# Kernel tuning notes

Hardware: AMD Instinct MI355X
Metric: run time of the kernel (lower is better)

## Reference

```python
import jax, jax.numpy as jnp
import numpy as np

A, B, I, H, O = 400, 64, 50, 192, 3   # num_agents, batch, input_dim, hidden_dim, output_dim
ADIM, NH = 128, 8                      # attention_dim, num_heads
HD = ADIM // NH
SCALE = HD ** -0.5
EPS = 1e-5


def _ln(x, g, b):
    mu = jnp.mean(x, -1, keepdims=True)
    v = jnp.mean((x - mu) ** 2, -1, keepdims=True)
    return (x - mu) * jax.lax.rsqrt(v + EPS) * g + b


def setup_inputs() -> dict:
    key = jax.random.key(0)
    ks = jax.random.split(key, 12)
    s = 0.05
    n = lambda k, shape: (jax.random.normal(k, shape, jnp.float32) * s)
    return {
        'x': jax.random.normal(ks[0], (B, I), jnp.float32),
        'ln_in_g': jnp.ones((A, I), jnp.float32), 'ln_in_b': jnp.zeros((A, I), jnp.float32),
        'W1': n(ks[1], (A, I, H)), 'b1': jnp.zeros((A, H), jnp.float32),
        'Ws1': n(ks[2], (A, I, H)), 'bs1': jnp.zeros((A, H), jnp.float32),
        'W2': n(ks[3], (A, H, H)), 'b2': jnp.zeros((A, H), jnp.float32),
        'Ws2': n(ks[4], (A, H, H)), 'bs2': jnp.zeros((A, H), jnp.float32),
        'W3': n(ks[5], (A, H, H)), 'b3': jnp.zeros((A, H), jnp.float32),
        'ln_h_g': jnp.ones((A, H), jnp.float32), 'ln_h_b': jnp.zeros((A, H), jnp.float32),
        'Wout': n(ks[6], (A, H, O)), 'bout': jnp.zeros((A, O), jnp.float32),
        'aln_g': jnp.ones((H,), jnp.float32), 'aln_b': jnp.zeros((H,), jnp.float32),
        'Wq': n(ks[7], (H, ADIM)), 'bq': jnp.zeros((ADIM,), jnp.float32),
        'Wk': n(ks[8], (H, ADIM)), 'bk': jnp.zeros((ADIM,), jnp.float32),
        'Wv': n(ks[9], (H, ADIM)), 'bv': jnp.zeros((ADIM,), jnp.float32),
        'Wo': n(ks[10], (ADIM, H)), 'bo': jnp.zeros((H,), jnp.float32),
    }


def _forward(x, ln_in_g, ln_in_b, W1, b1, Ws1, bs1, W2, b2, Ws2, bs2, W3, b3,
             ln_h_g, ln_h_b, Wout, bout, aln_g, aln_b, Wq, bq, Wk, bk, Wv, bv, Wo, bo):
    gelu = lambda t: jax.nn.gelu(t, approximate=False)  # torch F.gelu default = exact erf
    # per-agent input LayerNorm (shared stats, per-agent affine) -> [A, B, I]
    xn = _ln(x[None, :, :], ln_in_g[:, None, :], ln_in_b[:, None, :])
    # agent MLPs as batched GEMMs over agent axis
    h1 = gelu(jnp.einsum('abi,aih->abh', xn, W1) + b1[:, None, :]) \
         + jnp.einsum('abi,aih->abh', xn, Ws1) + bs1[:, None, :]
    h2 = gelu(jnp.einsum('abh,ahk->abk', h1, W2) + b2[:, None, :]) \
         + jnp.einsum('abh,ahk->abk', h1, Ws2) + bs2[:, None, :]
    h3 = _ln(h2 + jnp.einsum('abh,ahk->abk', h2, W3) + b3[:, None, :],
             ln_h_g[:, None, :], ln_h_b[:, None, :])  # [A, B, H]
    # cross-SREK attention across the agent axis
    y = _ln(h3, aln_g, aln_b)
    q = (y @ Wq + bq).reshape(A, B, NH, HD).transpose(1, 2, 0, 3)  # [B, NH, A, HD]
    k = (y @ Wk + bk).reshape(A, B, NH, HD).transpose(1, 2, 0, 3)
    v = (y @ Wv + bv).reshape(A, B, NH, HD).transpose(1, 2, 0, 3)
    attn = jax.nn.softmax(jnp.einsum('bhad,bhcd->bhac', q, k) * SCALE, axis=-1)
    o = jnp.einsum('bhac,bhcd->bhad', attn, v).transpose(2, 0, 1, 3).reshape(A, B, ADIM)
    attended = h3 + (o @ Wo + bo)  # residual (dropout off in eval)
    # per-agent output heads -> [A, B, O]
    logits = jnp.einsum('abh,aho->abo', attended, Wout) + bout[:, None, :]
    return logits


def reference(x, ln_in_g, ln_in_b, W1, b1, Ws1, bs1, W2, b2, Ws2, bs2, W3, b3,
              ln_h_g, ln_h_b, Wout, bout, aln_g, aln_b, Wq, bq, Wk, bk, Wv, bv, Wo, bo):
    return _forward(x, ln_in_g, ln_in_b, W1, b1, Ws1, bs1, W2, b2, Ws2, bs2, W3, b3,
                    ln_h_g, ln_h_b, Wout, bout, aln_g, aln_b, Wq, bq, Wk, bk, Wv, bv, Wo, bo)
```

## Files before the change

### kernel.cpp

```cpp
#include <hip/hip_runtime.h>
#include <math.h>

#define AGENTS 400
#define BATCH  64
#define IDIM   50
#define HDIM   192
#define ODIM   3
#define ADIMM  128
#define NHEADS 8
#define HEADD  16
#define LN_EPS 1e-5f

#define PA 200

typedef __bf16 bf16x8 __attribute__((ext_vector_type(8)));
typedef float  f32x4  __attribute__((ext_vector_type(4)));

__device__ __forceinline__ float gelu_exact(float x) {
    return 0.5f * x * (1.0f + erff(x * 0.70710678118654752f));
}

template<int NC, int KD, int NT, int LDW>
__device__ __forceinline__ void gemm_bpass(f32x4 (&acc)[4][NT],
                                           const float* const* wptr,
                                           const __bf16* Asrc, int lane)
{
    const int r = lane & 15, g = lane >> 4;
    float buf[2][NT * 8];

    #pragma unroll
    for (int t = 0; t < NT; t++)
        #pragma unroll
        for (int j = 0; j < 8; j++) {
            int k = g * 8 + j;
            buf[0][t * 8 + j] = (k < KD) ? wptr[t][k * LDW + r] : 0.f;
        }

    #pragma unroll
    for (int c = 0; c < NC; c++) {
        const int cur = c & 1, nxt = cur ^ 1;
        if (c + 1 < NC) {
            #pragma unroll
            for (int t = 0; t < NT; t++)
                #pragma unroll
                for (int j = 0; j < 8; j++) {
                    int k = (c + 1) * 32 + g * 8 + j;
                    buf[nxt][t * 8 + j] = (k < KD) ? wptr[t][k * LDW + r] : 0.f;
                }
        }
        bf16x8 bfr[NT];
        #pragma unroll
        for (int t = 0; t < NT; t++)
            #pragma unroll
            for (int j = 0; j < 8; j++)
                bfr[t][j] = (__bf16)buf[cur][t * 8 + j];
        #pragma unroll
        for (int rg = 0; rg < 4; rg++) {
            bf16x8 af = *(const bf16x8*)&Asrc[(16 * rg + r) * PA + c * 32 + g * 8];
            #pragma unroll
            for (int t = 0; t < NT; t++)
                acc[rg][t] = __builtin_amdgcn_mfma_f32_16x16x32_bf16(af, bfr[t], acc[rg][t], 0, 0, 0);
        }
    }
}

__global__ __launch_bounds__(256, 2) void mlp_kernel(
    const float* __restrict__ x,
    const float* __restrict__ ln_in_g, const float* __restrict__ ln_in_b,
    const float* __restrict__ W1, const float* __restrict__ b1,
    const float* __restrict__ Ws1, const float* __restrict__ bs1,
    const float* __restrict__ W2, const float* __restrict__ b2,
    const float* __restrict__ Ws2, const float* __restrict__ bs2,
    const float* __restrict__ W3, const float* __restrict__ b3,
    const float* __restrict__ ln_h_g, const float* __restrict__ ln_h_b,
    float* __restrict__ h3out)
{
    const int a    = blockIdx.x;
    const int tid  = threadIdx.x;
    const int wave = tid >> 6, lane = tid & 63;
    const int r = lane & 15, g = lane >> 4;
    const int n0 = 48 * wave;

    __shared__ __align__(16) __bf16 As[64 * PA];
    __shared__ float mu_s[64], rs_s[64];

    {
        int rr = tid >> 2, l = tid & 3;
        float s = 0.f, ss = 0.f;
        for (int k = l; k < IDIM; k += 4) { float v = x[rr * IDIM + k]; s += v; ss += v * v; }
        s  += __shfl_down(s, 2, 4);  s  += __shfl_down(s, 1, 4);
        ss += __shfl_down(ss, 2, 4); ss += __shfl_down(ss, 1, 4);
        if (l == 0) {
            float mu = s * (1.0f / IDIM);
            float var = ss * (1.0f / IDIM) - mu * mu;
            mu_s[rr] = mu;
            rs_s[rr] = rsqrtf(var + LN_EPS);
        }
    }
    __syncthreads();
    for (int sidx = tid; sidx < 64 * 64; sidx += 256) {
        int rr = sidx >> 6, k = sidx & 63;
        float v = 0.f;
        if (k < IDIM)
            v = (x[rr * IDIM + k] - mu_s[rr]) * rs_s[rr] * ln_in_g[a * IDIM + k] + ln_in_b[a * IDIM + k];
        As[rr * PA + k] = (__bf16)v;
    }
    __syncthreads();

    {
        f32x4 acc1[4][3], acc2[4][3];
        #pragma unroll
        for (int i = 0; i < 4; i++)
            #pragma unroll
            for (int t = 0; t < 3; t++) { acc1[i][t] = (f32x4)0.f; acc2[i][t] = (f32x4)0.f; }
        const float* W1p  = W1  + (size_t)a * IDIM * HDIM;
        const float* Ws1p = Ws1 + (size_t)a * IDIM * HDIM;
        const float* wA[3] = { W1p + n0,  W1p + n0 + 16,  W1p + n0 + 32 };
        const float* wB[3] = { Ws1p + n0, Ws1p + n0 + 16, Ws1p + n0 + 32 };
        gemm_bpass<2, IDIM, 3, HDIM>(acc1, wA, As, lane);
        gemm_bpass<2, IDIM, 3, HDIM>(acc2, wB, As, lane);
        __syncthreads();
        #pragma unroll
        for (int t = 0; t < 3; t++) {
            int col = n0 + 16 * t + r;
            float bb  = b1[a * HDIM + col];
            float bbs = bs1[a * HDIM + col];
            #pragma unroll
            for (int rg = 0; rg < 4; rg++)
                #pragma unroll
                for (int i = 0; i < 4; i++) {
                    int row = 16 * rg + 4 * g + i;
                    float v = gelu_exact(acc1[rg][t][i] + bb) + acc2[rg][t][i] + bbs;
                    As[row * PA + col] = (__bf16)v;
                }
        }
        __syncthreads();
    }

    {
        f32x4 acc1[4][3], acc2[4][3];
        #pragma unroll
        for (int i = 0; i < 4; i++)
            #pragma unroll
            for (int t = 0; t < 3; t++) { acc1[i][t] = (f32x4)0.f; acc2[i][t] = (f32x4)0.f; }
        const float* W2p  = W2  + (size_t)a * HDIM * HDIM;
        const float* Ws2p = Ws2 + (size_t)a * HDIM * HDIM;
        const float* wA[3] = { W2p + n0,  W2p + n0 + 16,  W2p + n0 + 32 };
        const float* wB[3] = { Ws2p + n0, Ws2p + n0 + 16, Ws2p + n0 + 32 };
        gemm_bpass<6, HDIM, 3, HDIM>(acc1, wA, As, lane);
        gemm_bpass<6, HDIM, 3, HDIM>(acc2, wB, As, lane);
        __syncthreads();
        #pragma unroll
        for (int t = 0; t < 3; t++) {
            int col = n0 + 16 * t + r;
            float bb  = b2[a * HDIM + col];
            float bbs = bs2[a * HDIM + col];
            #pragma unroll
            for (int rg = 0; rg < 4; rg++)
                #pragma unroll
                for (int i = 0; i < 4; i++) {
                    int row = 16 * rg + 4 * g + i;
                    float v = gelu_exact(acc1[rg][t][i] + bb) + acc2[rg][t][i] + bbs;
                    As[row * PA + col] = (__bf16)v;
                }
        }
        __syncthreads();
    }

    {
        f32x4 acc[4][3];
        #pragma unroll
        for (int i = 0; i < 4; i++)
            #pragma unroll
            for (int t = 0; t < 3; t++) acc[i][t] = (f32x4)0.f;
        const float* W3p = W3 + (size_t)a * HDIM * HDIM;
        const float* wA[3] = { W3p + n0, W3p + n0 + 16, W3p + n0 + 32 };
        gemm_bpass<6, HDIM, 3, HDIM>(acc, wA, As, lane);
        __syncthreads();
        #pragma unroll
        for (int t = 0; t < 3; t++) {
            int col = n0 + 16 * t + r;
            float bb = b3[a * HDIM + col];
            #pragma unroll
            for (int rg = 0; rg < 4; rg++)
                #pragma unroll
                for (int i = 0; i < 4; i++) {
                    int row = 16 * rg + 4 * g + i;
                    float v = (float)As[row * PA + col] + acc[rg][t][i] + bb;
                    As[row * PA + col] = (__bf16)v;
                }
        }
        __syncthreads();
    }

    {
        int rr = tid >> 2, l = tid & 3;
        float s = 0.f, ss = 0.f;
        for (int k = l; k < HDIM; k += 4) { float v = (float)As[rr * PA + k]; s += v; ss += v * v; }
        s  += __shfl_down(s, 2, 4);  s  += __shfl_down(s, 1, 4);
        ss += __shfl_down(ss, 2, 4); ss += __shfl_down(ss, 1, 4);
        if (l == 0) {
            float mu = s * (1.0f / HDIM);
            float var = ss * (1.0f / HDIM) - mu * mu;
            mu_s[rr] = mu;
            rs_s[rr] = rsqrtf(var + LN_EPS);
        }
    }
    __syncthreads();
    for (int sidx = tid; sidx < 64 * HDIM; sidx += 256) {
        int rr = sidx / HDIM, c = sidx - rr * HDIM;
        float v = ((float)As[rr * PA + c] - mu_s[rr]) * rs_s[rr] * ln_h_g[a * HDIM + c] + ln_h_b[a * HDIM + c];
        h3out[((size_t)a * BATCH + rr) * HDIM + c] = v;
    }
}

__global__ __launch_bounds__(256, 2) void qkv_kernel(
    const float* __restrict__ h3,
    const float* __restrict__ aln_g, const float* __restrict__ aln_b,
    const float* __restrict__ Wq, const float* __restrict__ bq,
    const float* __restrict__ Wk, const float* __restrict__ bk,
    const float* __restrict__ Wv, const float* __restrict__ bv,
    float* __restrict__ qT, float* __restrict__ kT, float* __restrict__ vT)
{
    const int a    = blockIdx.x;
    const int tid  = threadIdx.x;
    const int wave = tid >> 6, lane = tid & 63;
    const int r = lane & 15, g = lane >> 4;

    __shared__ __align__(16) __bf16 ys[64 * PA];
    __shared__ float mu_s[64], rs_s[64];

    {
        int rr = tid >> 2, l = tid & 3;
        const float* hp = h3 + ((size_t)a * BATCH + rr) * HDIM;
        float s = 0.f, ss = 0.f;
        for (int k = l; k < HDIM; k += 4) { float v = hp[k]; s += v; ss += v * v; }
        s  += __shfl_down(s, 2, 4);  s  += __shfl_down(s, 1, 4);
        ss += __shfl_down(ss, 2, 4); ss += __shfl_down(ss, 1, 4);
        if (l == 0) {
            float mu = s * (1.0f / HDIM);
            float var = ss * (1.0f / HDIM) - mu * mu;
            mu_s[rr] = mu;
            rs_s[rr] = rsqrtf(var + LN_EPS);
        }
    }
    __syncthreads();
    for (int sidx = tid; sidx < 64 * HDIM; sidx += 256) {
        int rr = sidx / HDIM, c = sidx - rr * HDIM;
        float v = (h3[((size_t)a * BATCH + rr) * HDIM + c] - mu_s[rr]) * rs_s[rr] * aln_g[c] + aln_b[c];
        ys[rr * PA + c] = (__bf16)v;
    }
    __syncthreads();

    #pragma unroll
    for (int p = 0; p < 2; p++) {
        const int nb = 192 * p + 48 * wave;
        const float* wA[3];
        #pragma unroll
        for (int t = 0; t < 3; t++) {
            int nt = nb + 16 * t;
            const float* base = (nt < 128) ? Wq : (nt < 256) ? Wk : Wv;
            wA[t] = base + (nt & 127);
        }
        f32x4 acc[4][3];
        #pragma unroll
        for (int i = 0; i < 4; i++)
            #pragma unroll
            for (int t = 0; t < 3; t++) acc[i][t] = (f32x4)0.f;
        gemm_bpass<6, HDIM, 3, ADIMM>(acc, wA, ys, lane);

        #pragma unroll
        for (int t = 0; t < 3; t++) {
            int n = nb + 16 * t + r;
            int which = n >> 7, cc = n & 127, hh = cc >> 4, dd = cc & 15;
            const float* bp = (which == 0) ? bq : (which == 1) ? bk : bv;
            float* op = (which == 0) ? qT : (which == 1) ? kT : vT;
            float bb = bp[cc];
            #pragma unroll
            for (int rg = 0; rg < 4; rg++)
                #pragma unroll
                for (int i = 0; i < 4; i++) {
                    int brow = 16 * rg + 4 * g + i;
                    op[(((size_t)brow * NHEADS + hh) * AGENTS + a) * HEADD + dd] = acc[rg][t][i] + bb;
                }
        }
    }
}

#define PKA 24
#define PVA 408
#define PPA 232

__global__ __launch_bounds__(256, 2) void attn_kernel(
    const float* __restrict__ qT, const float* __restrict__ kT,
    const float* __restrict__ vT, float* __restrict__ oT)
{
    const int bh   = blockIdx.x;
    const int tid  = threadIdx.x;
    const int wave = tid >> 6, lane = tid & 63;
    const int r = lane & 15, g = lane >> 4;

    __shared__ __align__(16) __bf16 Ks[AGENTS * PKA];
    __shared__ __align__(16) __bf16 Vt[16 * PVA];
    __shared__ __align__(16) __bf16 Ps[4][16 * PPA];

    const float* kp = kT + (size_t)bh * AGENTS * HEADD;
    const float* vp = vT + (size_t)bh * AGENTS * HEADD;
    for (int idx = tid; idx < AGENTS * HEADD; idx += 256) {
        int a_ = idx >> 4, d = idx & 15;
        Ks[a_ * PKA + d] = (__bf16)kp[idx];
        Vt[d * PVA + a_] = (__bf16)vp[idx];
    }
    __bf16* Pw = Ps[wave];
    for (int z = lane; z < 16 * 16; z += 64)
        Pw[(z >> 4) * PPA + 208 + (z & 15)] = (__bf16)0.f;
    __syncthreads();

    for (int mt = wave; mt < 25; mt += 4) {
        const int m0 = mt * 16;

        bf16x8 aq;
        if (g < 2) {
            const float* qp = qT + ((size_t)bh * AGENTS + m0 + r) * HEADD + g * 8;
            #pragma unroll
            for (int j = 0; j < 8; j++) aq[j] = (__bf16)(qp[j] * 0.25f);
        } else {
            #pragma unroll
            for (int j = 0; j < 8; j++) aq[j] = (__bf16)0.f;
        }

        f32x4 sacc[25];
        #pragma unroll
        for (int t = 0; t < 25; t++) {
            bf16x8 bk_ = *(const bf16x8*)&Ks[(t * 16 + r) * PKA + (g & 1) * 8];
            sacc[t] = __builtin_amdgcn_mfma_f32_16x16x32_bf16(aq, bk_, (f32x4)0.f, 0, 0, 0);
        }

        float lv[4];
        #pragma unroll
        for (int i = 0; i < 4; i++) {
            float m_ = sacc[0][i];
            #pragma unroll
            for (int t = 1; t < 25; t++) m_ = fmaxf(m_, sacc[t][i]);
            #pragma unroll
            for (int off = 8; off; off >>= 1) m_ = fmaxf(m_, __shfl_xor(m_, off, 16));
            float l_ = 0.f;
            #pragma unroll
            for (int t = 0; t < 25; t++) {
                float p = __expf(sacc[t][i] - m_);
                sacc[t][i] = p;
                l_ += p;
            }
            #pragma unroll
            for (int off = 8; off; off >>= 1) l_ += __shfl_xor(l_, off, 16);
            lv[i] = l_;
        }

        f32x4 oacc = (f32x4)0.f;

        #pragma unroll
        for (int t = 0; t < 13; t++)
            #pragma unroll
            for (int i = 0; i < 4; i++)
                Pw[(g * 4 + i) * PPA + t * 16 + r] = (__bf16)sacc[t][i];
        __asm__ volatile("s_waitcnt lgkmcnt(0)" ::: "memory");
        #pragma unroll
        for (int c = 0; c < 7; c++) {
            bf16x8 ap  = *(const bf16x8*)&Pw[r * PPA + c * 32 + g * 8];
            bf16x8 bv_ = *(const bf16x8*)&Vt[r * PVA + c * 32 + g * 8];
            oacc = __builtin_amdgcn_mfma_f32_16x16x32_bf16(ap, bv_, oacc, 0, 0, 0);
        }

        for (int z = lane; z < 16 * 16; z += 64)
            Pw[(z >> 4) * PPA + 192 + (z & 15)] = (__bf16)0.f;
        #pragma unroll
        for (int t = 13; t < 25; t++)
            #pragma unroll
            for (int i = 0; i < 4; i++)
                Pw[(g * 4 + i) * PPA + (t - 13) * 16 + r] = (__bf16)sacc[t][i];
        __asm__ volatile("s_waitcnt lgkmcnt(0)" ::: "memory");
        #pragma unroll
        for (int c = 0; c < 6; c++) {
            bf16x8 ap  = *(const bf16x8*)&Pw[r * PPA + c * 32 + g * 8];
            bf16x8 bv_ = *(const bf16x8*)&Vt[r * PVA + 208 + c * 32 + g * 8];
            oacc = __builtin_amdgcn_mfma_f32_16x16x32_bf16(ap, bv_, oacc, 0, 0, 0);
        }

        float* op = oT + ((size_t)bh * AGENTS + m0) * HEADD;
        #pragma unroll
        for (int i = 0; i < 4; i++)
            op[(g * 4 + i) * HEADD + r] = oacc[i] / lv[i];
    }
}

__global__ __launch_bounds__(256) void out_kernel(
    const float* __restrict__ h3, const float* __restrict__ oT,
    const float* __restrict__ Wo, const float* __restrict__ bo,
    const float* __restrict__ Wout, const float* __restrict__ bout,
    float* __restrict__ out)
{
    const int a      = blockIdx.x;
    const int r_base = blockIdx.y * 32;
    const int tid    = threadIdx.x;
    __shared__ float os[32][ADIMM + 1];
    __shared__ float att[32][HDIM + 1];

    for (int idx = tid; idx < 32 * HDIM; idx += 256) {
        int rr = idx / HDIM, c = idx - rr * HDIM;
        att[rr][c] = h3[((size_t)a * BATCH + (r_base + rr)) * HDIM + c];
    }
    for (int idx = tid; idx < 32 * ADIMM; idx += 256) {
        int rr = idx >> 7, j = idx & 127;
        int h = j >> 4, d = j & 15;
        int b = r_base + rr;
        os[rr][j] = oT[(((size_t)b * NHEADS + h) * AGENTS + a) * HEADD + d];
    }
    __syncthreads();

    const int cx = tid & 63;
    const int rg = (tid >> 6) * 8;
    {
        float acc[3][8];
        #pragma unroll
        for (int m = 0; m < 3; m++)
            #pragma unroll
            for (int rr = 0; rr < 8; rr++) acc[m][rr] = 0.f;
        for (int k = 0; k < ADIMM; k++) {
            float w[3];
            #pragma unroll
            for (int m = 0; m < 3; m++) w[m] = Wo[k * HDIM + cx + 64 * m];
            #pragma unroll
            for (int rr = 0; rr < 8; rr++) {
                float ov = os[rg + rr][k];
                #pragma unroll
                for (int m = 0; m < 3; m++) acc[m][rr] = fmaf(ov, w[m], acc[m][rr]);
            }
        }
        #pragma unroll
        for (int m = 0; m < 3; m++) {
            int c = cx + 64 * m;
            float bb = bo[c];
            #pragma unroll
            for (int rr = 0; rr < 8; rr++)
                att[rg + rr][c] += acc[m][rr] + bb;
        }
    }
    __syncthreads();

    if (tid < 32 * ODIM) {
        int rr = tid & 31;
        int c = tid >> 5;
        const float* Wp = Wout + (size_t)a * HDIM * ODIM;
        float accv = 0.f;
        for (int k = 0; k < HDIM; k++)
            accv = fmaf(att[rr][k], Wp[k * ODIM + c], accv);
        out[((size_t)a * BATCH + (r_base + rr)) * ODIM + c] = accv + bout[a * ODIM + c];
    }
}

extern "C" void kernel_launch(void* const* d_in, const int* in_sizes, int n_in,
                              void* d_out, int out_size, void* d_ws, size_t ws_size,
                              hipStream_t stream)
{
    const float* x       = (const float*)d_in[0];
    const float* ln_in_g = (const float*)d_in[1];
    const float* ln_in_b = (const float*)d_in[2];
    const float* W1      = (const float*)d_in[3];
    const float* b1      = (const float*)d_in[4];
    const float* Ws1     = (const float*)d_in[5];
    const float* bs1     = (const float*)d_in[6];
    const float* W2      = (const float*)d_in[7];
    const float* b2      = (const float*)d_in[8];
    const float* Ws2     = (const float*)d_in[9];
    const float* bs2     = (const float*)d_in[10];
    const float* W3      = (const float*)d_in[11];
    const float* b3      = (const float*)d_in[12];
    const float* ln_h_g  = (const float*)d_in[13];
    const float* ln_h_b  = (const float*)d_in[14];
    const float* Wout    = (const float*)d_in[15];
    const float* bout    = (const float*)d_in[16];
    const float* aln_g   = (const float*)d_in[17];
    const float* aln_b   = (const float*)d_in[18];
    const float* Wq      = (const float*)d_in[19];
    const float* bq      = (const float*)d_in[20];
    const float* Wk      = (const float*)d_in[21];
    const float* bk      = (const float*)d_in[22];
    const float* Wv      = (const float*)d_in[23];
    const float* bv      = (const float*)d_in[24];
    const float* Wo      = (const float*)d_in[25];
    const float* bo      = (const float*)d_in[26];
    float* out = (float*)d_out;

    float* ws = (float*)d_ws;
    const size_t H3_SZ = (size_t)AGENTS * BATCH * HDIM;
    const size_t QT_SZ = (size_t)BATCH * NHEADS * AGENTS * HEADD;
    float* h3 = ws;
    float* qT = h3 + H3_SZ;
    float* kT = qT + QT_SZ;
    float* vT = kT + QT_SZ;
    float* oT = vT + QT_SZ;

    mlp_kernel<<<AGENTS, 256, 0, stream>>>(x, ln_in_g, ln_in_b,
                                           W1, b1, Ws1, bs1, W2, b2, Ws2, bs2,
                                           W3, b3, ln_h_g, ln_h_b, h3);
    qkv_kernel<<<AGENTS, 256, 0, stream>>>(h3, aln_g, aln_b,
                                           Wq, bq, Wk, bk, Wv, bv, qT, kT, vT);
    attn_kernel<<<BATCH * NHEADS, 256, 0, stream>>>(qT, kT, vT, oT);
    out_kernel<<<dim3(AGENTS, 2), 256, 0, stream>>>(h3, oT, Wo, bo, Wout, bout, out);
}
```

Before: 400.7 us.

## Double waves per block in MLP/QKV and move output projection to MFMA

The MLP and QKV kernels now launch 512 threads, splitting the 64 batch rows into two halves across wave pairs, so each wave holds half the accumulators and more waves hide weight-load latency. The attention kernel now writes its output in agent-major [A,B,ADIM] order so the output kernel can read contiguous rows. The output kernel is rewritten to do the Wo projection and the per-agent Wout head with bf16 MFMA instead of scalar FMA loops, using one block per agent. Each weight tile is now loaded by twice as many waves, and the extra bf16 rounding of the residual before the head may cost some accuracy.

```diff
diff --git a/kernel.cpp b/kernel.cpp
--- a/kernel.cpp
+++ b/kernel.cpp
@@ -11,7 +11,8 @@
 #define HEADD  16
 #define LN_EPS 1e-5f
 
-#define PA 200
+#define PA   200
+#define POUT 136
 
 typedef __bf16 bf16x8 __attribute__((ext_vector_type(8)));
 typedef float  f32x4  __attribute__((ext_vector_type(4)));
@@ -20,8 +21,14 @@
     return 0.5f * x * (1.0f + erff(x * 0.70710678118654752f));
 }
 
-template<int NC, int KD, int NT, int LDW>
-__device__ __forceinline__ void gemm_bpass(f32x4 (&acc)[4][NT],
+__device__ __forceinline__ unsigned pack_bf16x2(float a, float b) {
+    unsigned short ua = __builtin_bit_cast(unsigned short, (__bf16)a);
+    unsigned short ub = __builtin_bit_cast(unsigned short, (__bf16)b);
+    return (unsigned)ua | ((unsigned)ub << 16);
+}
+
+template<int NC, int KD, int NT, int NRG, int LDW, int PITCH>
+__device__ __forceinline__ void gemm_bpass(f32x4 (&acc)[NRG][NT],
                                            const float* const* wptr,
                                            const __bf16* Asrc, int lane)
 {
@@ -55,8 +62,8 @@
             for (int j = 0; j < 8; j++)
                 bfr[t][j] = (__bf16)buf[cur][t * 8 + j];
         #pragma unroll
-        for (int rg = 0; rg < 4; rg++) {
-            bf16x8 af = *(const bf16x8*)&Asrc[(16 * rg + r) * PA + c * 32 + g * 8];
+        for (int rg = 0; rg < NRG; rg++) {
+            bf16x8 af = *(const bf16x8*)&Asrc[(16 * rg + r) * PITCH + c * 32 + g * 8];
             #pragma unroll
             for (int t = 0; t < NT; t++)
                 acc[rg][t] = __builtin_amdgcn_mfma_f32_16x16x32_bf16(af, bfr[t], acc[rg][t], 0, 0, 0);
@@ -64,7 +71,7 @@
     }
 }
 
-__global__ __launch_bounds__(256, 2) void mlp_kernel(
+__global__ __launch_bounds__(512, 4) void mlp_kernel(
     const float* __restrict__ x,
     const float* __restrict__ ln_in_g, const float* __restrict__ ln_in_b,
     const float* __restrict__ W1, const float* __restrict__ b1,
@@ -79,17 +86,23 @@
     const int tid  = threadIdx.x;
     const int wave = tid >> 6, lane = tid & 63;
     const int r = lane & 15, g = lane >> 4;
-    const int n0 = 48 * wave;
+    const int cg = wave & 3, mh = wave >> 2;
+    const int n0 = 48 * cg;
+    const __bf16* Aw;
 
     __shared__ __align__(16) __bf16 As[64 * PA];
     __shared__ float mu_s[64], rs_s[64];
-
-    {
-        int rr = tid >> 2, l = tid & 3;
+    Aw = As + 32 * mh * PA;
+
+    {
+        int rr = tid >> 3, l = tid & 7;
         float s = 0.f, ss = 0.f;
-        for (int k = l; k < IDIM; k += 4) { float v = x[rr * IDIM + k]; s += v; ss += v * v; }
-        s  += __shfl_down(s, 2, 4);  s  += __shfl_down(s, 1, 4);
-        ss += __shfl_down(ss, 2, 4); ss += __shfl_down(ss, 1, 4);
+        for (int k = l; k < IDIM; k += 8) { float v = x[rr * IDIM + k]; s += v; ss += v * v; }
+        #pragma unroll
+        for (int off = 4; off; off >>= 1) {
+            s  += __shfl_down(s,  off, 8);
+            ss += __shfl_down(ss, off, 8);
+        }
         if (l == 0) {
             float mu = s * (1.0f / IDIM);
             float var = ss * (1.0f / IDIM) - mu * mu;
@@ -98,7 +111,7 @@
         }
     }
     __syncthreads();
-    for (int sidx = tid; sidx < 64 * 64; sidx += 256) {
+    for (int sidx = tid; sidx < 64 * 64; sidx += 512) {
         int rr = sidx >> 6, k = sidx & 63;
         float v = 0.f;
         if (k < IDIM)
@@ -108,17 +121,22 @@
     __syncthreads();
 
     {
-        f32x4 acc1[4][3], acc2[4][3];
-        #pragma unroll
-        for (int i = 0; i < 4; i++)
-            #pragma unroll
-            for (int t = 0; t < 3; t++) { acc1[i][t] = (f32x4)0.f; acc2[i][t] = (f32x4)0.f; }
         const float* W1p  = W1  + (size_t)a * IDIM * HDIM;
         const float* Ws1p = Ws1 + (size_t)a * IDIM * HDIM;
         const float* wA[3] = { W1p + n0,  W1p + n0 + 16,  W1p + n0 + 32 };
         const float* wB[3] = { Ws1p + n0, Ws1p + n0 + 16, Ws1p + n0 + 32 };
-        gemm_bpass<2, IDIM, 3, HDIM>(acc1, wA, As, lane);
-        gemm_bpass<2, IDIM, 3, HDIM>(acc2, wB, As, lane);
+        f32x4 acc1[2][3];
+        #pragma unroll
+        for (int i = 0; i < 2; i++)
+            #pragma unroll
+            for (int t = 0; t < 3; t++) acc1[i][t] = (f32x4)0.f;
+        gemm_bpass<2, IDIM, 3, 2, HDIM, PA>(acc1, wA, Aw, lane);
+        f32x4 acc2[2][3];
+        #pragma unroll
+        for (int i = 0; i < 2; i++)
+            #pragma unroll
+            for (int t = 0; t < 3; t++) acc2[i][t] = (f32x4)0.f;
+        gemm_bpass<2, IDIM, 3, 2, HDIM, PA>(acc2, wB, Aw, lane);
         __syncthreads();
         #pragma unroll
         for (int t = 0; t < 3; t++) {
@@ -126,10 +144,10 @@
             float bb  = b1[a * HDIM + col];
             float bbs = bs1[a * HDIM + col];
             #pragma unroll
-            for (int rg = 0; rg < 4; rg++)
+            for (int rg = 0; rg < 2; rg++)
                 #pragma unroll
                 for (int i = 0; i < 4; i++) {
-                    int row = 16 * rg + 4 * g + i;
+                    int row = 32 * mh + 16 * rg + 4 * g + i;
                     float v = gelu_exact(acc1[rg][t][i] + bb) + acc2[rg][t][i] + bbs;
                     As[row * PA + col] = (__bf16)v;
                 }
@@ -138,17 +156,22 @@
     }
 
     {
-        f32x4 acc1[4][3], acc2[4][3];
-        #pragma unroll
-        for (int i = 0; i < 4; i++)
-            #pragma unroll
-            for (int t = 0; t < 3; t++) { acc1[i][t] = (f32x4)0.f; acc2[i][t] = (f32x4)0.f; }
         const float* W2p  = W2  + (size_t)a * HDIM * HDIM;
         const float* Ws2p = Ws2 + (size_t)a * HDIM * HDIM;
         const float* wA[3] = { W2p + n0,  W2p + n0 + 16,  W2p + n0 + 32 };
         const float* wB[3] = { Ws2p + n0, Ws2p + n0 + 16, Ws2p + n0 + 32 };
-        gemm_bpass<6, HDIM, 3, HDIM>(acc1, wA, As, lane);
-        gemm_bpass<6, HDIM, 3, HDIM>(acc2, wB, As, lane);
+        f32x4 acc1[2][3];
+        #pragma unroll
+        for (int i = 0; i < 2; i++)
+            #pragma unroll
+            for (int t = 0; t < 3; t++) acc1[i][t] = (f32x4)0.f;
+        gemm_bpass<6, HDIM, 3, 2, HDIM, PA>(acc1, wA, Aw, lane);
+        f32x4 acc2[2][3];
+        #pragma unroll
+        for (int i = 0; i < 2; i++)
+            #pragma unroll
+            for (int t = 0; t < 3; t++) acc2[i][t] = (f32x4)0.f;
+        gemm_bpass<6, HDIM, 3, 2, HDIM, PA>(acc2, wB, Aw, lane);
         __syncthreads();
         #pragma unroll
         for (int t = 0; t < 3; t++) {
@@ -156,10 +179,10 @@
             float bb  = b2[a * HDIM + col];
             float bbs = bs2[a * HDIM + col];
             #pragma unroll
-            for (int rg = 0; rg < 4; rg++)
+            for (int rg = 0; rg < 2; rg++)
                 #pragma unroll
                 for (int i = 0; i < 4; i++) {
-                    int row = 16 * rg + 4 * g + i;
+                    int row = 32 * mh + 16 * rg + 4 * g + i;
                     float v = gelu_exact(acc1[rg][t][i] + bb) + acc2[rg][t][i] + bbs;
                     As[row * PA + col] = (__bf16)v;
                 }
@@ -168,24 +191,24 @@
     }
 
     {
-        f32x4 acc[4][3];
-        #pragma unroll
-        for (int i = 0; i < 4; i++)
-            #pragma unroll
-            for (int t = 0; t < 3; t++) acc[i][t] = (f32x4)0.f;
         const float* W3p = W3 + (size_t)a * HDIM * HDIM;
         const float* wA[3] = { W3p + n0, W3p + n0 + 16, W3p + n0 + 32 };
-        gemm_bpass<6, HDIM, 3, HDIM>(acc, wA, As, lane);
+        f32x4 acc[2][3];
+        #pragma unroll
+        for (int i = 0; i < 2; i++)
+            #pragma unroll
+            for (int t = 0; t < 3; t++) acc[i][t] = (f32x4)0.f;
+        gemm_bpass<6, HDIM, 3, 2, HDIM, PA>(acc, wA, Aw, lane);
         __syncthreads();
         #pragma unroll
         for (int t = 0; t < 3; t++) {
             int col = n0 + 16 * t + r;
             float bb = b3[a * HDIM + col];
             #pragma unroll
-            for (int rg = 0; rg < 4; rg++)
+            for (int rg = 0; rg < 2; rg++)
                 #pragma unroll
                 for (int i = 0; i < 4; i++) {
-                    int row = 16 * rg + 4 * g + i;
+                    int row = 32 * mh + 16 * rg + 4 * g + i;
                     float v = (float)As[row * PA + col] + acc[rg][t][i] + bb;
                     As[row * PA + col] = (__bf16)v;
                 }
@@ -194,11 +217,14 @@
     }
 
     {
-        int rr = tid >> 2, l = tid & 3;
+        int rr = tid >> 3, l = tid & 7;
         float s = 0.f, ss = 0.f;
-        for (int k = l; k < HDIM; k += 4) { float v = (float)As[rr * PA + k]; s += v; ss += v * v; }
-        s  += __shfl_down(s, 2, 4);  s  += __shfl_down(s, 1, 4);
-        ss += __shfl_down(ss, 2, 4); ss += __shfl_down(ss, 1, 4);
+        for (int k = l; k < HDIM; k += 8) { float v = (float)As[rr * PA + k]; s += v; ss += v * v; }
+        #pragma unroll
+        for (int off = 4; off; off >>= 1) {
+            s  += __shfl_down(s,  off, 8);
+            ss += __shfl_down(ss, off, 8);
+        }
         if (l == 0) {
             float mu = s * (1.0f / HDIM);
             float var = ss * (1.0f / HDIM) - mu * mu;
@@ -207,14 +233,14 @@
         }
     }
     __syncthreads();
-    for (int sidx = tid; sidx < 64 * HDIM; sidx += 256) {
+    for (int sidx = tid; sidx < 64 * HDIM; sidx += 512) {
         int rr = sidx / HDIM, c = sidx - rr * HDIM;
         float v = ((float)As[rr * PA + c] - mu_s[rr]) * rs_s[rr] * ln_h_g[a * HDIM + c] + ln_h_b[a * HDIM + c];
         h3out[((size_t)a * BATCH + rr) * HDIM + c] = v;
     }
 }
 
-__global__ __launch_bounds__(256, 2) void qkv_kernel(
+__global__ __launch_bounds__(512, 4) void qkv_kernel(
     const float* __restrict__ h3,
     const float* __restrict__ aln_g, const float* __restrict__ aln_b,
     const float* __restrict__ Wq, const float* __restrict__ bq,
@@ -226,17 +252,22 @@
     const int tid  = threadIdx.x;
     const int wave = tid >> 6, lane = tid & 63;
     const int r = lane & 15, g = lane >> 4;
+    const int cg = wave & 3, mh = wave >> 2;
 
     __shared__ __align__(16) __bf16 ys[64 * PA];
     __shared__ float mu_s[64], rs_s[64];
-
-    {
-        int rr = tid >> 2, l = tid & 3;
+    const __bf16* Aw = ys + 32 * mh * PA;
+
+    {
+        int rr = tid >> 3, l = tid & 7;
         const float* hp = h3 + ((size_t)a * BATCH + rr) * HDIM;
         float s = 0.f, ss = 0.f;
-        for (int k = l; k < HDIM; k += 4) { float v = hp[k]; s += v; ss += v * v; }
-        s  += __shfl_down(s, 2, 4);  s  += __shfl_down(s, 1, 4);
-        ss += __shfl_down(ss, 2, 4); ss += __shfl_down(ss, 1, 4);
+        for (int k = l; k < HDIM; k += 8) { float v = hp[k]; s += v; ss += v * v; }
+        #pragma unroll
+        for (int off = 4; off; off >>= 1) {
+            s  += __shfl_down(s,  off, 8);
+            ss += __shfl_down(ss, off, 8);
+        }
         if (l == 0) {
             float mu = s * (1.0f / HDIM);
             float var = ss * (1.0f / HDIM) - mu * mu;
@@ -245,7 +276,7 @@
         }
     }
     __syncthreads();
-    for (int sidx = tid; sidx < 64 * HDIM; sidx += 256) {
+    for (int sidx = tid; sidx < 64 * HDIM; sidx += 512) {
         int rr = sidx / HDIM, c = sidx - rr * HDIM;
         float v = (h3[((size_t)a * BATCH + rr) * HDIM + c] - mu_s[rr]) * rs_s[rr] * aln_g[c] + aln_b[c];
         ys[rr * PA + c] = (__bf16)v;
@@ -254,7 +285,7 @@
 
     #pragma unroll
     for (int p = 0; p < 2; p++) {
-        const int nb = 192 * p + 48 * wave;
+        const int nb = 192 * p + 48 * cg;
         const float* wA[3];
         #pragma unroll
         for (int t = 0; t < 3; t++) {
@@ -262,12 +293,12 @@
             const float* base = (nt < 128) ? Wq : (nt < 256) ? Wk : Wv;
             wA[t] = base + (nt & 127);
         }
-        f32x4 acc[4][3];
-        #pragma unroll
-        for (int i = 0; i < 4; i++)
+        f32x4 acc[2][3];
+        #pragma unroll
+        for (int i = 0; i < 2; i++)
             #pragma unroll
             for (int t = 0; t < 3; t++) acc[i][t] = (f32x4)0.f;
-        gemm_bpass<6, HDIM, 3, ADIMM>(acc, wA, ys, lane);
+        gemm_bpass<6, HDIM, 3, 2, ADIMM, PA>(acc, wA, Aw, lane);
 
         #pragma unroll
         for (int t = 0; t < 3; t++) {
@@ -277,10 +308,10 @@
             float* op = (which == 0) ? qT : (which == 1) ? kT : vT;
             float bb = bp[cc];
             #pragma unroll
-            for (int rg = 0; rg < 4; rg++)
+            for (int rg = 0; rg < 2; rg++)
                 #pragma unroll
                 for (int i = 0; i < 4; i++) {
-                    int brow = 16 * rg + 4 * g + i;
+                    int brow = 32 * mh + 16 * rg + 4 * g + i;
                     op[(((size_t)brow * NHEADS + hh) * AGENTS + a) * HEADD + dd] = acc[rg][t][i] + bb;
                 }
         }
@@ -296,6 +327,7 @@
     const float* __restrict__ vT, float* __restrict__ oT)
 {
     const int bh   = blockIdx.x;
+    const int b    = bh >> 3, h = bh & 7;
     const int tid  = threadIdx.x;
     const int wave = tid >> 6, lane = tid & 63;
     const int r = lane & 15, g = lane >> 4;
@@ -386,75 +418,87 @@
             oacc = __builtin_amdgcn_mfma_f32_16x16x32_bf16(ap, bv_, oacc, 0, 0, 0);
         }
 
-        float* op = oT + ((size_t)bh * AGENTS + m0) * HEADD;
         #pragma unroll
         for (int i = 0; i < 4; i++)
-            op[(g * 4 + i) * HEADD + r] = oacc[i] / lv[i];
-    }
-}
-
-__global__ __launch_bounds__(256) void out_kernel(
+            oT[((size_t)(m0 + g * 4 + i) * BATCH + b) * ADIMM + h * HEADD + r] = oacc[i] / lv[i];
+    }
+}
+
+__global__ __launch_bounds__(256, 2) void out_kernel(
     const float* __restrict__ h3, const float* __restrict__ oT,
     const float* __restrict__ Wo, const float* __restrict__ bo,
     const float* __restrict__ Wout, const float* __restrict__ bout,
     float* __restrict__ out)
 {
-    const int a      = blockIdx.x;
-    const int r_base = blockIdx.y * 32;
-    const int tid    = threadIdx.x;
-    __shared__ float os[32][ADIMM + 1];
-    __shared__ float att[32][HDIM + 1];
-
-    for (int idx = tid; idx < 32 * HDIM; idx += 256) {
-        int rr = idx / HDIM, c = idx - rr * HDIM;
-        att[rr][c] = h3[((size_t)a * BATCH + (r_base + rr)) * HDIM + c];
-    }
-    for (int idx = tid; idx < 32 * ADIMM; idx += 256) {
-        int rr = idx >> 7, j = idx & 127;
-        int h = j >> 4, d = j & 15;
-        int b = r_base + rr;
-        os[rr][j] = oT[(((size_t)b * NHEADS + h) * AGENTS + a) * HEADD + d];
-    }
-    __syncthreads();
-
-    const int cx = tid & 63;
-    const int rg = (tid >> 6) * 8;
-    {
-        float acc[3][8];
-        #pragma unroll
-        for (int m = 0; m < 3; m++)
-            #pragma unroll
-            for (int rr = 0; rr < 8; rr++) acc[m][rr] = 0.f;
-        for (int k = 0; k < ADIMM; k++) {
-            float w[3];
-            #pragma unroll
-            for (int m = 0; m < 3; m++) w[m] = Wo[k * HDIM + cx + 64 * m];
-            #pragma unroll
-            for (int rr = 0; rr < 8; rr++) {
-                float ov = os[rg + rr][k];
+    const int a    = blockIdx.x;
+    const int tid  = threadIdx.x;
+    const int wave = tid >> 6, lane = tid & 63;
+    const int r = lane & 15, g = lane >> 4;
+    const int n0 = 48 * wave;
+
+    __shared__ __align__(16) __bf16 os[64 * POUT];
+    __shared__ __align__(16) __bf16 att[64 * PA];
+
+    for (int idx = tid; idx < 64 * 32; idx += 256) {
+        int bb = idx >> 5, q = idx & 31;
+        float4 v = ((const float4*)(oT + ((size_t)a * BATCH + bb) * ADIMM))[q];
+        unsigned u0 = pack_bf16x2(v.x, v.y);
+        unsigned u1 = pack_bf16x2(v.z, v.w);
+        *(uint2*)&os[bb * POUT + q * 4] = make_uint2(u0, u1);
+    }
+    __syncthreads();
+
+    {
+        const float* wA[3] = { Wo + n0, Wo + n0 + 16, Wo + n0 + 32 };
+        f32x4 acc[4][3];
+        #pragma unroll
+        for (int i = 0; i < 4; i++)
+            #pragma unroll
+            for (int t = 0; t < 3; t++) acc[i][t] = (f32x4)0.f;
+        gemm_bpass<4, ADIMM, 3, 4, HDIM, POUT>(acc, wA, os, lane);
+        #pragma unroll
+        for (int t = 0; t < 3; t++) {
+            int col = n0 + 16 * t + r;
+            float bb = bo[col];
+            #pragma unroll
+            for (int rg = 0; rg < 4; rg++)
                 #pragma unroll
-                for (int m = 0; m < 3; m++) acc[m][rr] = fmaf(ov, w[m], acc[m][rr]);
+                for (int i = 0; i < 4; i++) {
+                    int row = 16 * rg + 4 * g + i;
+                    float v = h3[((size_t)a * BATCH + row) * HDIM + col] + acc[rg][t][i] + bb;
+                    att[row * PA + col] = (__bf16)v;
+                }
+        }
+    }
+    __syncthreads();
+
+    {
+        const float* Wp = Wout + (size_t)a * HDIM * ODIM;
+        float wb[48];
+        #pragma unroll
+        for (int c = 0; c < 6; c++)
+            #pragma unroll
+            for (int j = 0; j < 8; j++) {
+                int k = c * 32 + g * 8 + j;
+                wb[c * 8 + j] = (r < ODIM) ? Wp[k * ODIM + r] : 0.f;
             }
-        }
-        #pragma unroll
-        for (int m = 0; m < 3; m++) {
-            int c = cx + 64 * m;
-            float bb = bo[c];
-            #pragma unroll
-            for (int rr = 0; rr < 8; rr++)
-                att[rg + rr][c] += acc[m][rr] + bb;
-        }
-    }
-    __syncthreads();
-
-    if (tid < 32 * ODIM) {
-        int rr = tid & 31;
-        int c = tid >> 5;
-        const float* Wp = Wout + (size_t)a * HDIM * ODIM;
-        float accv = 0.f;
-        for (int k = 0; k < HDIM; k++)
-            accv = fmaf(att[rr][k], Wp[k * ODIM + c], accv);
-        out[((size_t)a * BATCH + (r_base + rr)) * ODIM + c] = accv + bout[a * ODIM + c];
+        f32x4 oacc = (f32x4)0.f;
+        #pragma unroll
+        for (int c = 0; c < 6; c++) {
+            bf16x8 bf;
+            #pragma unroll
+            for (int j = 0; j < 8; j++) bf[j] = (__bf16)wb[c * 8 + j];
+            bf16x8 af = *(const bf16x8*)&att[(16 * wave + r) * PA + c * 32 + g * 8];
+            oacc = __builtin_amdgcn_mfma_f32_16x16x32_bf16(af, bf, oacc, 0, 0, 0);
+        }
+        if (r < ODIM) {
+            float bb = bout[a * ODIM + r];
+            #pragma unroll
+            for (int i = 0; i < 4; i++) {
+                int row = 16 * wave + 4 * g + i;
+                out[((size_t)a * BATCH + row) * ODIM + r] = oacc[i] + bb;
+            }
+        }
     }
 }
 
@@ -500,11 +544,11 @@
     float* vT = kT + QT_SZ;
     float* oT = vT + QT_SZ;
 
-    mlp_kernel<<<AGENTS, 256, 0, stream>>>(x, ln_in_g, ln_in_b,
+    mlp_kernel<<<AGENTS, 512, 0, stream>>>(x, ln_in_g, ln_in_b,
                                            W1, b1, Ws1, bs1, W2, b2, Ws2, bs2,
                                            W3, b3, ln_h_g, ln_h_b, h3);
-    qkv_kernel<<<AGENTS, 256, 0, stream>>>(h3, aln_g, aln_b,
+    qkv_kernel<<<AGENTS, 512, 0, stream>>>(h3, aln_g, aln_b,
                                            Wq, bq, Wk, bk, Wv, bv, qT, kT, vT);
     attn_kernel<<<BATCH * NHEADS, 256, 0, stream>>>(qT, kT, vT, oT);
-    out_kernel<<<dim3(AGENTS, 2), 256, 0, stream>>>(h3, oT, Wo, bo, Wout, bout, out);
-}
+    out_kernel<<<AGENTS, 256, 0, stream>>>(h3, oT, Wo, bo, Wout, bout, out);
+}
```

Result: slower. 435.3 us (+8.6%).
